# Kernel tuning notes

Hardware: AMD Instinct MI355X
Metric: run time of the kernel (lower is better)

Reference implementation:

```python
import jax, jax.numpy as jnp
import numpy as np

D_MODEL = 1024
N_HEAD = 16


def setup_inputs() -> dict:
    key = jax.random.key(0)
    ks = jax.random.split(key, 12)
    B, T, D = 2, 2048, D_MODEL
    s = 1.0 / np.sqrt(D)
    return {
        "q": jax.random.normal(ks[0], (B, T, D), jnp.float32),
        "k": jax.random.normal(ks[1], (B, T, D), jnp.float32),
        "v": jax.random.normal(ks[2], (B, T, D), jnp.float32),
        "w_q": jax.random.normal(ks[3], (D, D), jnp.float32) * s,
        "b_q": jnp.zeros((D,), jnp.float32),
        "w_k": jax.random.normal(ks[4], (D, D), jnp.float32) * s,
        "b_k": jnp.zeros((D,), jnp.float32),
        "w_v": jax.random.normal(ks[5], (D, D), jnp.float32) * s,
        "b_v": jnp.zeros((D,), jnp.float32),
        "w_o": jax.random.normal(ks[6], (D, D), jnp.float32) * s,
        "b_o": jnp.zeros((D,), jnp.float32),
    }


def reference(q, k, v, w_q, b_q, w_k, b_k, w_v, b_v, w_o, b_o):
    B, T, D = q.shape
    H = N_HEAD
    nd = D // H  # head dim
    # projections (weights stored as [in, out])
    qh = (q @ w_q + b_q).reshape(B, T, H, nd).transpose(0, 2, 1, 3)  # [b,h,t,nd]
    kh = (k @ w_k + b_k).reshape(B, T, H, nd).transpose(0, 2, 1, 3)
    vh = (v @ w_v + b_v).reshape(B, T, H, nd).transpose(0, 2, 1, 3)
    score = jnp.einsum('bhqd,bhkd->bhqk', qh, kh) / jnp.sqrt(jnp.float32(nd))
    causal = jnp.tril(jnp.ones((T, T), dtype=bool))  # [tq, tk]
    score = jnp.where(causal, score, -jnp.inf)
    # NOTE: original module uses nn.Softmax(dim=-2), i.e. softmax over the
    # QUERY axis. Faithful to the source.
    attn = jax.nn.softmax(score, axis=-2)
    out = jnp.einsum('bhqk,bhkd->bhqd', attn, vh)  # [b,h,t,nd]
    out = out.transpose(0, 2, 1, 3).reshape(B, T, D)
    return out @ w_o + b_o
```

## Files before the change

kernel.cpp:

```cpp
#include <hip/hip_runtime.h>
#include <hip/hip_bf16.h>
#include <cstdint>
#include <cstddef>

#define D_MODEL 1024
#define NHEAD   16
#define HDIM    64
#define BB      2
#define TT      2048
#define MM      (BB*TT)
#define BHN     (BB*NHEAD)

typedef __attribute__((ext_vector_type(8))) __bf16 bf16x8;
typedef __attribute__((ext_vector_type(4))) float  f32x4;
typedef __attribute__((ext_vector_type(8))) unsigned short u16x8;
typedef __attribute__((ext_vector_type(4))) unsigned short u16x4;

__device__ __forceinline__ unsigned short f2b(float f){
  __bf16 b = (__bf16)f;
  return __builtin_bit_cast(unsigned short, b);
}

__device__ __forceinline__ f32x4 mfma16(bf16x8 a, bf16x8 b, f32x4 c){
  return __builtin_amdgcn_mfma_f32_16x16x32_bf16(a, b, c, 0, 0, 0);
}

__device__ __forceinline__ void gload16(const void* g, void* lds){
  __builtin_amdgcn_global_load_lds((const __attribute__((address_space(1))) void*)g,
                                   (__attribute__((address_space(3))) void*)lds, 16, 0, 0);
}

__global__ void pre_kernel(const float* __restrict__ q, const float* __restrict__ k,
                           const float* __restrict__ v,
                           unsigned short* __restrict__ Xq, unsigned short* __restrict__ Xk,
                           unsigned short* __restrict__ Xv,
                           const float* __restrict__ W0, const float* __restrict__ W1,
                           const float* __restrict__ W2, const float* __restrict__ W3,
                           unsigned short* __restrict__ T0, unsigned short* __restrict__ T1,
                           unsigned short* __restrict__ T2, unsigned short* __restrict__ T3)
{
  __shared__ float tile[32][33];
  const int id = blockIdx.x;
  if (id < 6144){
    const int z = id / 2048, ib = id - z*2048;
    const float* x = z==0 ? q : z==1 ? k : v;
    unsigned short* y = z==0 ? Xq : z==1 ? Xk : Xv;
    size_t i = (size_t)ib*256 + threadIdx.x;
    const float4* p = (const float4*)(x + i*8);
    float4 a = p[0], b = p[1];
    u16x8 o;
    o[0]=f2b(a.x); o[1]=f2b(a.y); o[2]=f2b(a.z); o[3]=f2b(a.w);
    o[4]=f2b(b.x); o[5]=f2b(b.y); o[6]=f2b(b.z); o[7]=f2b(b.w);
    *(u16x8*)(y + i*8) = o;
  } else {
    const int tid = id - 6144;
    const int z = tid >> 10;
    const int by = (tid >> 5) & 31, bx = tid & 31;
    const float* W = z==0 ? W0 : z==1 ? W1 : z==2 ? W2 : W3;
    unsigned short* Wt = z==0 ? T0 : z==1 ? T1 : z==2 ? T2 : T3;
    const int tx = threadIdx.x & 31, ty = threadIdx.x >> 5;
    const int x0 = bx*32, y0 = by*32;
    #pragma unroll
    for (int i=0;i<4;i++)
      tile[ty + i*8][tx] = W[(size_t)(y0 + ty + i*8)*D_MODEL + x0 + tx];
    __syncthreads();
    #pragma unroll
    for (int i=0;i<4;i++)
      Wt[(size_t)(x0 + ty + i*8)*D_MODEL + y0 + tx] = f2b(tile[tx][ty + i*8]);
  }
}

__device__ __forceinline__ void gemm_body(const unsigned short* __restrict__ A,
                                          const unsigned short* __restrict__ Bt,
                                          const float* __restrict__ bias,
                                          void* __restrict__ Cout, const int mode,
                                          const int m0, const int n0)
{
  constexpr int K = D_MODEL, N = D_MODEL;
  __shared__ unsigned short As[2][128*32];
  __shared__ unsigned short Bs[2][128*32];
  const int t = threadIdx.x, lane = t&63, w = t>>6;
  const int wr = w>>1, wc = w&1, lr = lane&15, lg = lane>>4;
  const int srow = lane>>2;
  const int schunk = (lane&3) ^ ((lane>>3)&3);
  const int crd = lg ^ ((lr>>1)&3);
  f32x4 acc[4][4] = {};

  auto stage = [&](int buf, int k0){
    #pragma unroll
    for (int g=0; g<2; g++){
      int reg = w*2 + g;
      int r = reg*16 + srow;
      gload16(A  + (size_t)(m0+r)*K + k0 + schunk*8, (char*)As[buf] + reg*1024);
      gload16(Bt + (size_t)(n0+r)*K + k0 + schunk*8, (char*)Bs[buf] + reg*1024);
    }
  };

  stage(0, 0);
  __syncthreads();
  int buf = 0;
  for (int ks = 0; ks < 32; ++ks){
    if (ks < 31) stage(buf^1, (ks+1)*32);
    const char* bufA = (const char*)As[buf];
    const char* bufB = (const char*)Bs[buf];
    bf16x8 af[4], bfv[4];
    #pragma unroll
    for (int mi=0;mi<4;mi++){
      int r = wr*64 + mi*16 + lr;
      af[mi] = *(const bf16x8*)(bufA + r*64 + crd*16);
    }
    #pragma unroll
    for (int ni=0;ni<4;ni++){
      int r = wc*64 + ni*16 + lr;
      bfv[ni] = *(const bf16x8*)(bufB + r*64 + crd*16);
    }
    #pragma unroll
    for (int mi=0;mi<4;mi++)
      #pragma unroll
      for (int ni=0;ni<4;ni++)
        acc[mi][ni] = mfma16(af[mi], bfv[ni], acc[mi][ni]);
    __syncthreads();
    buf ^= 1;
  }

  #pragma unroll
  for (int mi=0;mi<4;mi++){
    #pragma unroll
    for (int ni=0;ni<4;ni++){
      int n = n0 + wc*64 + ni*16 + lr;
      int mbase = m0 + wr*64 + mi*16 + lg*4;
      float bv = bias[n];
      if (mode == 0){
        unsigned short* Cb = (unsigned short*)Cout;
        #pragma unroll
        for (int r=0;r<4;r++) Cb[(size_t)(mbase+r)*N + n] = f2b(acc[mi][ni][r] + bv);
      } else {
        unsigned short* Vt = (unsigned short*)Cout;
        int h = n >> 6, d = n & 63;
        int b = mbase >> 11;
        int tq = mbase & (TT-1);
        u16x4 vv;
        #pragma unroll
        for (int r=0;r<4;r++) vv[r] = f2b(acc[mi][ni][r] + bv);
        *(u16x4*)(Vt + ((size_t)((b*NHEAD + h)*HDIM + d))*TT + tq) = vv;
      }
    }
  }
}

__launch_bounds__(256)
__global__ void proj_gemm_kernel(const unsigned short* __restrict__ Xq,
                                 const unsigned short* __restrict__ Xk,
                                 const unsigned short* __restrict__ Xv,
                                 const unsigned short* __restrict__ Wtq,
                                 const unsigned short* __restrict__ Wtk,
                                 const unsigned short* __restrict__ Wtv,
                                 const float* __restrict__ b_q, const float* __restrict__ b_k,
                                 const float* __restrict__ b_v,
                                 unsigned short* __restrict__ Qb, unsigned short* __restrict__ Kb,
                                 unsigned short* __restrict__ Vt)
{
  const int id = blockIdx.x;
  const int xcd = id & 7, r2 = id >> 3;
  const int n = r2 & 7, mz = r2 >> 3;
  const int m = (mz & 3)*8 + xcd, z = mz >> 2;
  const unsigned short* A  = z==0 ? Xq : z==1 ? Xk : Xv;
  const unsigned short* Bt = z==0 ? Wtq : z==1 ? Wtk : Wtv;
  const float* bias = z==0 ? b_q : z==1 ? b_k : b_v;
  void* C = z==0 ? (void*)Qb : z==1 ? (void*)Kb : (void*)Vt;
  gemm_body(A, Bt, bias, C, z==2 ? 1 : 0, m*128, n*128);
}

__launch_bounds__(256)
__global__ void out_gemm_kernel(const unsigned short* __restrict__ Ob,
                                const unsigned short* __restrict__ Wto,
                                const float* __restrict__ b_o, float* __restrict__ out)
{
  constexpr int K = D_MODEL, N = D_MODEL;
  __shared__ unsigned short As[2][64*32];
  __shared__ unsigned short Bs[2][128*32];
  const int id = blockIdx.x;
  const int xcd = id & 7, r2 = id >> 3;
  const int n0 = (r2 & 7)*128, m0 = ((r2 >> 3)*8 + xcd)*64;
  const int t = threadIdx.x, lane = t&63, w = t>>6;
  const int wr = w>>1, wc = w&1, lr = lane&15, lg = lane>>4;
  const int srow = lane>>2;
  const int schunk = (lane&3) ^ ((lane>>3)&3);
  const int crd = lg ^ ((lr>>1)&3);
  f32x4 acc[2][4] = {};

  auto stage = [&](int buf, int k0){
    { int r = w*16 + srow;
      gload16(Ob + (size_t)(m0+r)*K + k0 + schunk*8, (char*)As[buf] + w*1024); }
    #pragma unroll
    for (int g=0; g<2; g++){
      int reg = w*2 + g;
      int r = reg*16 + srow;
      gload16(Wto + (size_t)(n0+r)*K + k0 + schunk*8, (char*)Bs[buf] + reg*1024);
    }
  };

  stage(0, 0);
  __syncthreads();
  int buf = 0;
  for (int ks = 0; ks < 32; ++ks){
    if (ks < 31) stage(buf^1, (ks+1)*32);
    const char* bufA = (const char*)As[buf];
    const char* bufB = (const char*)Bs[buf];
    bf16x8 af[2], bfv[4];
    #pragma unroll
    for (int mi=0;mi<2;mi++){
      int r = wr*32 + mi*16 + lr;
      af[mi] = *(const bf16x8*)(bufA + r*64 + crd*16);
    }
    #pragma unroll
    for (int ni=0;ni<4;ni++){
      int r = wc*64 + ni*16 + lr;
      bfv[ni] = *(const bf16x8*)(bufB + r*64 + crd*16);
    }
    #pragma unroll
    for (int mi=0;mi<2;mi++)
      #pragma unroll
      for (int ni=0;ni<4;ni++)
        acc[mi][ni] = mfma16(af[mi], bfv[ni], acc[mi][ni]);
    __syncthreads();
    buf ^= 1;
  }

  #pragma unroll
  for (int mi=0;mi<2;mi++){
    #pragma unroll
    for (int ni=0;ni<4;ni++){
      int n = n0 + wc*64 + ni*16 + lr;
      int mbase = m0 + wr*32 + mi*16 + lg*4;
      float bv = b_o[n];
      #pragma unroll
      for (int r=0;r<4;r++) out[(size_t)(mbase+r)*N + n] = acc[mi][ni][r] + bv;
    }
  }
}

__launch_bounds__(256)
__global__ void col_stats_kernel(const unsigned short* __restrict__ Qb,
                                 const unsigned short* __restrict__ Kb,
                                 float* __restrict__ partialS)
{
  __shared__ unsigned short Ks[128*64];
  __shared__ unsigned short Qs[2][64*64];
  const int t = threadIdx.x, lane = t&63, w = t>>6;
  const int id = blockIdx.x;
  const int bh = id & 31, pair = id >> 5;
  const int kb_ = pair & 15, qc = pair >> 4;
  const int b = bh >> 4, h = bh & 15;
  const int k0 = kb_ * 128;
  const int lr = lane&15, lg = lane>>4;
  const int osrc = (lane&7) ^ (lane>>3);

  auto stageQ = [&](int buf, int qt){
    #pragma unroll
    for (int g=0; g<2; g++){
      int reg = w*2 + g;
      int r = reg*8 + (lane>>3);
      gload16(Qb + ((size_t)(b*TT + qt + r))*D_MODEL + h*64 + osrc*8,
              (char*)Qs[buf] + reg*1024);
    }
  };

  const int qstart = (k0 > qc*256) ? k0 : qc*256;
  const int qend   = (qc+1)*256;

  #pragma unroll
  for (int g=0; g<4; g++){
    int reg = w*4 + g;
    int r = reg*8 + (lane>>3);
    gload16(Kb + ((size_t)(b*TT + k0 + r))*D_MODEL + h*64 + osrc*8, (char*)Ks + reg*1024);
  }
  if (qstart < qend) stageQ(0, qstart);
  __syncthreads();

  bf16x8 bk[2][2];
  #pragma unroll
  for (int kb=0;kb<2;kb++)
    #pragma unroll
    for (int ks=0;ks<2;ks++){
      int r = w*32 + kb*16 + lr;
      bk[kb][ks] = *(const bf16x8*)((const char*)Ks + r*128 + (((ks*4+lg) ^ (r&7))*16));
    }
  f32x4 sacc[2] = {};
  int buf = 0;
  for (int qt = qstart; qt < qend; qt += 64){
    if (qt + 64 < qend) stageQ(buf^1, qt+64);
    const char* bufQ = (const char*)Qs[buf];
    const bool interior = (qt >= k0 + 128);
    #pragma unroll
    for (int qb=0;qb<4;qb++){
      bf16x8 aq[2];
      #pragma unroll
      for (int ks=0;ks<2;ks++){
        int r = qb*16 + lr;
        aq[ks] = *(const bf16x8*)(bufQ + r*128 + (((ks*4+lg) ^ (r&7))*16));
      }
      f32x4 sf[2] = {};
      #pragma unroll
      for (int ks=0;ks<2;ks++)
        #pragma unroll
        for (int kb=0;kb<2;kb++)
          sf[kb] = mfma16(aq[ks], bk[kb][ks], sf[kb]);
      #pragma unroll
      for (int kb=0;kb<2;kb++){
        int col = k0 + w*32 + kb*16 + lr;
        #pragma unroll
        for (int r=0;r<4;r++){
          float e = __expf(sf[kb][r] * 0.125f);
          if (!interior){
            int qg = qt + qb*16 + lg*4 + r;
            e = (qg >= col) ? e : 0.f;
          }
          sacc[kb][r] += e;
        }
      }
    }
    __syncthreads();
    buf ^= 1;
  }
  #pragma unroll
  for (int kb=0;kb<2;kb++){
    float s = sacc[kb][0] + sacc[kb][1] + sacc[kb][2] + sacc[kb][3];
    s += __shfl_xor(s, 16);
    s += __shfl_xor(s, 32);
    if (lg == 0){
      int col = k0 + w*32 + kb*16 + lr;
      partialS[((size_t)qc*BHN + bh)*TT + col] = s;
    }
  }
}

__launch_bounds__(512)
__global__ void attn_out_kernel(const unsigned short* __restrict__ Qb,
                                const unsigned short* __restrict__ Kb,
                                const unsigned short* __restrict__ Vt,
                                const float* __restrict__ partialS,
                                unsigned short* __restrict__ O)
{
  __shared__ unsigned short Qs[128*64];
  __shared__ unsigned short Ks2[2][64*64];
  __shared__ unsigned short Vs[2][64*64];
  __shared__ unsigned short Ps[128*64];
  __shared__ float inv_s[TT];
  const int t = threadIdx.x, lane=t&63, w=t>>6;
  const int id = blockIdx.x;
  const int bh = id & 31;
  const int qi = 15 - (id >> 5);
  const int b = bh>>4, h = bh&15;
  const int q0 = qi*128;
  const int lr = lane&15, lg = lane>>4;
  const int osrc = (lane&7) ^ (lane>>3);

  auto stageKV = [&](int buf, int k0){
    int r = w*8 + (lane>>3);
    gload16(Kb + ((size_t)(b*TT + k0 + r))*D_MODEL + h*64 + osrc*8,
            (char*)Ks2[buf] + w*1024);
    gload16(Vt + ((size_t)(bh*HDIM + r))*TT + k0 + osrc*8,
            (char*)Vs[buf] + w*1024);
  };

  #pragma unroll
  for (int g=0; g<2; g++){
    int reg = w*2 + g;
    int r = reg*8 + (lane>>3);
    gload16(Qb + ((size_t)(b*TT + q0 + r))*D_MODEL + h*64 + osrc*8, (char*)Qs + reg*1024);
  }
  stageKV(0, 0);

  const int ncols = q0 + 128;
  for (int c = t; c < ncols; c += 512){
    float s = 0.f;
    #pragma unroll
    for (int qc=0;qc<8;qc++) s += partialS[((size_t)qc*BHN + bh)*TT + c];
    inv_s[c] = 1.0f / s;
  }
  __syncthreads();

  bf16x8 aq[2];
  #pragma unroll
  for (int ks=0;ks<2;ks++){
    int r = w*16 + lr;
    aq[ks] = *(const bf16x8*)((const char*)Qs + r*128 + (((ks*4+lg) ^ (r&7))*16));
  }
  f32x4 oacc[4] = {};
  const int nkt = 2*qi + 2;
  int buf = 0;
  for (int kt=0; kt<nkt; kt++){
    int k0 = kt*64;
    if (kt+1 < nkt) stageKV(buf^1, k0+64);
    const bool active = (k0 <= q0 + w*16 + 15);
    if (active){
      const char* bufK = (const char*)Ks2[buf];
      const char* bufV = (const char*)Vs[buf];
      f32x4 sf[4] = {};
      __builtin_amdgcn_s_setprio(1);
      #pragma unroll
      for (int ks=0;ks<2;ks++)
        #pragma unroll
        for (int kb=0;kb<4;kb++){
          int r = kb*16 + lr;
          bf16x8 bk = *(const bf16x8*)(bufK + r*128 + (((ks*4+lg) ^ (r&7))*16));
          sf[kb] = mfma16(bk, aq[ks], sf[kb]);
        }
      __builtin_amdgcn_s_setprio(0);
      const bool boundary = (k0 + 64 > q0 + w*16);
      const int prow = w*16 + lr;
      #pragma unroll
      for (int kb=0;kb<4;kb++){
        f32x4 inv4 = *(const f32x4*)&inv_s[k0 + kb*16 + lg*4];
        u16x4 vv;
        #pragma unroll
        for (int r=0;r<4;r++){
          float pv = __expf(sf[kb][r]*0.125f) * inv4[r];
          if (boundary){
            int kg = k0 + kb*16 + lg*4 + r;
            int qg = q0 + prow;
            pv = (qg >= kg) ? pv : 0.f;
          }
          vv[r] = f2b(pv);
        }
        *(u16x4*)((char*)Ps + ((prow*128 + kb*32 + lg*8) ^ ((prow&7)<<4))) = vv;
      }
      __builtin_amdgcn_s_setprio(1);
      #pragma unroll
      for (int ks=0;ks<2;ks++){
        bf16x8 pa = *(const bf16x8*)((const char*)Ps + prow*128 + (((ks*4+lg) ^ (prow&7))*16));
        #pragma unroll
        for (int db=0;db<4;db++){
          int r = db*16 + lr;
          bf16x8 bv = *(const bf16x8*)(bufV + r*128 + (((ks*4+lg) ^ (r&7))*16));
          oacc[db] = mfma16(pa, bv, oacc[db]);
        }
      }
      __builtin_amdgcn_s_setprio(0);
    }
    __syncthreads();
    buf ^= 1;
  }
  #pragma unroll
  for (int db=0;db<4;db++){
    int qg = q0 + w*16 + lg*4;
    int d  = db*16 + lr;
    #pragma unroll
    for (int r=0;r<4;r++)
      O[((size_t)(b*TT + qg + r))*D_MODEL + h*64 + d] = f2b(oacc[db][r]);
  }
}

extern "C" void kernel_launch(void* const* d_in, const int* in_sizes, int n_in,
                              void* d_out, int out_size, void* d_ws, size_t ws_size,
                              hipStream_t stream)
{
  (void)in_sizes; (void)n_in; (void)out_size; (void)ws_size;
  const float* q   = (const float*)d_in[0];
  const float* k   = (const float*)d_in[1];
  const float* v   = (const float*)d_in[2];
  const float* w_q = (const float*)d_in[3];
  const float* b_q = (const float*)d_in[4];
  const float* w_k = (const float*)d_in[5];
  const float* b_k = (const float*)d_in[6];
  const float* w_v = (const float*)d_in[7];
  const float* b_v = (const float*)d_in[8];
  const float* w_o = (const float*)d_in[9];
  const float* b_o = (const float*)d_in[10];

  char* p = (char*)d_ws;
  auto carve = [&](size_t bytes)->char* {
    char* r = p; p += (bytes + 255) & ~(size_t)255; return r;
  };
  unsigned short* Xq  = (unsigned short*)carve((size_t)MM*D_MODEL*2);
  unsigned short* Xk  = (unsigned short*)carve((size_t)MM*D_MODEL*2);
  unsigned short* Xv  = (unsigned short*)carve((size_t)MM*D_MODEL*2);
  unsigned short* Wtq = (unsigned short*)carve((size_t)D_MODEL*D_MODEL*2);
  unsigned short* Wtk = (unsigned short*)carve((size_t)D_MODEL*D_MODEL*2);
  unsigned short* Wtv = (unsigned short*)carve((size_t)D_MODEL*D_MODEL*2);
  unsigned short* Wto = (unsigned short*)carve((size_t)D_MODEL*D_MODEL*2);
  unsigned short* Qb  = (unsigned short*)carve((size_t)MM*D_MODEL*2);
  unsigned short* Kb  = (unsigned short*)carve((size_t)MM*D_MODEL*2);
  unsigned short* Vt  = (unsigned short*)carve((size_t)MM*D_MODEL*2);
  unsigned short* Ob  = (unsigned short*)carve((size_t)MM*D_MODEL*2);
  float* partialS = (float*)carve((size_t)8*BHN*TT*4);

  pre_kernel<<<dim3(6144 + 4096), 256, 0, stream>>>(q, k, v, Xq, Xk, Xv,
                                                    w_q, w_k, w_v, w_o,
                                                    Wtq, Wtk, Wtv, Wto);

  proj_gemm_kernel<<<dim3(768), 256, 0, stream>>>(Xq, Xk, Xv, Wtq, Wtk, Wtv,
                                                  b_q, b_k, b_v, Qb, Kb, Vt);

  col_stats_kernel<<<dim3(8*16*BHN), 256, 0, stream>>>(Qb, Kb, partialS);

  attn_out_kernel<<<dim3((TT/128)*BHN), 512, 0, stream>>>(Qb, Kb, Vt, partialS, Ob);

  out_gemm_kernel<<<dim3(512), 256, 0, stream>>>(Ob, Wto, b_o, (float*)d_out);
}
```

Baseline: 142.6 us.

## Pair causal query strips per block for balanced attention and fold score scale into Q

The attention-output kernel now gives each 256-thread block two 64-row query strips, one near the start and its mirror near the end, so every block covers the same number of causal key tiles and shares each staged K/V tile between both strips. The 1/sqrt(d) scale is applied once when Q is written in the projection GEMM, which removes a multiply from the exp in both the column-stats and attention kernels. This trades 512-thread blocks with idle warps for balanced smaller blocks. It also rounds the scaled Q to bf16, which changes numerics slightly.

```diff
diff --git a/kernel.cpp b/kernel.cpp
--- a/kernel.cpp
+++ b/kernel.cpp
@@ -74,7 +74,7 @@
                                           const unsigned short* __restrict__ Bt,
                                           const float* __restrict__ bias,
                                           void* __restrict__ Cout, const int mode,
-                                          const int m0, const int n0)
+                                          const int m0, const int n0, const float oscale)
 {
   constexpr int K = D_MODEL, N = D_MODEL;
   __shared__ unsigned short As[2][128*32];
@@ -133,7 +133,7 @@
       if (mode == 0){
         unsigned short* Cb = (unsigned short*)Cout;
         #pragma unroll
-        for (int r=0;r<4;r++) Cb[(size_t)(mbase+r)*N + n] = f2b(acc[mi][ni][r] + bv);
+        for (int r=0;r<4;r++) Cb[(size_t)(mbase+r)*N + n] = f2b((acc[mi][ni][r] + bv)*oscale);
       } else {
         unsigned short* Vt = (unsigned short*)Cout;
         int h = n >> 6, d = n & 63;
@@ -168,7 +168,7 @@
   const unsigned short* Bt = z==0 ? Wtq : z==1 ? Wtk : Wtv;
   const float* bias = z==0 ? b_q : z==1 ? b_k : b_v;
   void* C = z==0 ? (void*)Qb : z==1 ? (void*)Kb : (void*)Vt;
-  gemm_body(A, Bt, bias, C, z==2 ? 1 : 0, m*128, n*128);
+  gemm_body(A, Bt, bias, C, z==2 ? 1 : 0, m*128, n*128, z==0 ? 0.125f : 1.0f);
 }
 
 __launch_bounds__(256)
@@ -311,7 +311,7 @@
         int col = k0 + w*32 + kb*16 + lr;
         #pragma unroll
         for (int r=0;r<4;r++){
-          float e = __expf(sf[kb][r] * 0.125f);
+          float e = __expf(sf[kb][r]);
           if (!interior){
             int qg = qt + qb*16 + lg*4 + r;
             e = (qg >= col) ? e : 0.f;
@@ -335,45 +335,55 @@
   }
 }
 
-__launch_bounds__(512)
+__launch_bounds__(256)
 __global__ void attn_out_kernel(const unsigned short* __restrict__ Qb,
                                 const unsigned short* __restrict__ Kb,
                                 const unsigned short* __restrict__ Vt,
                                 const float* __restrict__ partialS,
                                 unsigned short* __restrict__ O)
 {
-  __shared__ unsigned short Qs[128*64];
+  __shared__ unsigned short Qs[2][64*64];
   __shared__ unsigned short Ks2[2][64*64];
   __shared__ unsigned short Vs[2][64*64];
-  __shared__ unsigned short Ps[128*64];
+  __shared__ unsigned short Ps[64*64];
   __shared__ float inv_s[TT];
   const int t = threadIdx.x, lane=t&63, w=t>>6;
   const int id = blockIdx.x;
   const int bh = id & 31;
-  const int qi = 15 - (id >> 5);
+  const int pr = id >> 5;
   const int b = bh>>4, h = bh&15;
-  const int q0 = qi*128;
+  const int q0A = pr*64, q0B = (31-pr)*64;
+  const int nkt = (31-pr) + 1;
   const int lr = lane&15, lg = lane>>4;
   const int osrc = (lane&7) ^ (lane>>3);
 
+  auto stageQ = [&](int s, int q0){
+    #pragma unroll
+    for (int g=0; g<2; g++){
+      int reg = w*2 + g;
+      int r = reg*8 + (lane>>3);
+      gload16(Qb + ((size_t)(b*TT + q0 + r))*D_MODEL + h*64 + osrc*8,
+              (char*)Qs[s] + reg*1024);
+    }
+  };
   auto stageKV = [&](int buf, int k0){
-    int r = w*8 + (lane>>3);
-    gload16(Kb + ((size_t)(b*TT + k0 + r))*D_MODEL + h*64 + osrc*8,
-            (char*)Ks2[buf] + w*1024);
-    gload16(Vt + ((size_t)(bh*HDIM + r))*TT + k0 + osrc*8,
-            (char*)Vs[buf] + w*1024);
-  };
-
-  #pragma unroll
-  for (int g=0; g<2; g++){
-    int reg = w*2 + g;
-    int r = reg*8 + (lane>>3);
-    gload16(Qb + ((size_t)(b*TT + q0 + r))*D_MODEL + h*64 + osrc*8, (char*)Qs + reg*1024);
-  }
+    #pragma unroll
+    for (int g=0; g<2; g++){
+      int reg = w*2 + g;
+      int r = reg*8 + (lane>>3);
+      gload16(Kb + ((size_t)(b*TT + k0 + r))*D_MODEL + h*64 + osrc*8,
+              (char*)Ks2[buf] + reg*1024);
+      gload16(Vt + ((size_t)(bh*HDIM + r))*TT + k0 + osrc*8,
+              (char*)Vs[buf] + reg*1024);
+    }
+  };
+
+  stageQ(0, q0A);
+  stageQ(1, q0B);
   stageKV(0, 0);
 
-  const int ncols = q0 + 128;
-  for (int c = t; c < ncols; c += 512){
+  const int ncols = nkt*64;
+  for (int c = t; c < ncols; c += 256){
     float s = 0.f;
     #pragma unroll
     for (int qc=0;qc<8;qc++) s += partialS[((size_t)qc*BHN + bh)*TT + c];
@@ -381,74 +391,81 @@
   }
   __syncthreads();
 
-  bf16x8 aq[2];
+  bf16x8 aqA[2], aqB[2];
   #pragma unroll
   for (int ks=0;ks<2;ks++){
     int r = w*16 + lr;
-    aq[ks] = *(const bf16x8*)((const char*)Qs + r*128 + (((ks*4+lg) ^ (r&7))*16));
-  }
-  f32x4 oacc[4] = {};
-  const int nkt = 2*qi + 2;
+    aqA[ks] = *(const bf16x8*)((const char*)Qs[0] + r*128 + (((ks*4+lg) ^ (r&7))*16));
+    aqB[ks] = *(const bf16x8*)((const char*)Qs[1] + r*128 + (((ks*4+lg) ^ (r&7))*16));
+  }
+  f32x4 oaccA[4] = {}, oaccB[4] = {};
+  const int prow = w*16 + lr;
+
+  auto strip_step = [&](const bf16x8* aq, f32x4* oacc, int q0, int k0,
+                        const char* bufK, const char* bufV){
+    f32x4 sf[4] = {};
+    __builtin_amdgcn_s_setprio(1);
+    #pragma unroll
+    for (int ks=0;ks<2;ks++)
+      #pragma unroll
+      for (int kb=0;kb<4;kb++){
+        int r = kb*16 + lr;
+        bf16x8 bk = *(const bf16x8*)(bufK + r*128 + (((ks*4+lg) ^ (r&7))*16));
+        sf[kb] = mfma16(bk, aq[ks], sf[kb]);
+      }
+    __builtin_amdgcn_s_setprio(0);
+    const bool boundary = (k0 + 64 > q0 + w*16);
+    #pragma unroll
+    for (int kb=0;kb<4;kb++){
+      f32x4 inv4 = *(const f32x4*)&inv_s[k0 + kb*16 + lg*4];
+      u16x4 vv;
+      #pragma unroll
+      for (int r=0;r<4;r++){
+        float pv = __expf(sf[kb][r]) * inv4[r];
+        if (boundary){
+          int kg = k0 + kb*16 + lg*4 + r;
+          pv = (q0 + prow >= kg) ? pv : 0.f;
+        }
+        vv[r] = f2b(pv);
+      }
+      *(u16x4*)((char*)Ps + ((prow*128 + kb*32 + lg*8) ^ ((prow&7)<<4))) = vv;
+    }
+    __builtin_amdgcn_s_setprio(1);
+    #pragma unroll
+    for (int ks=0;ks<2;ks++){
+      bf16x8 pa = *(const bf16x8*)((const char*)Ps + prow*128 + (((ks*4+lg) ^ (prow&7))*16));
+      #pragma unroll
+      for (int db=0;db<4;db++){
+        int r = db*16 + lr;
+        bf16x8 bv = *(const bf16x8*)(bufV + r*128 + (((ks*4+lg) ^ (r&7))*16));
+        oacc[db] = mfma16(pa, bv, oacc[db]);
+      }
+    }
+    __builtin_amdgcn_s_setprio(0);
+  };
+
   int buf = 0;
   for (int kt=0; kt<nkt; kt++){
     int k0 = kt*64;
     if (kt+1 < nkt) stageKV(buf^1, k0+64);
-    const bool active = (k0 <= q0 + w*16 + 15);
-    if (active){
-      const char* bufK = (const char*)Ks2[buf];
-      const char* bufV = (const char*)Vs[buf];
-      f32x4 sf[4] = {};
-      __builtin_amdgcn_s_setprio(1);
-      #pragma unroll
-      for (int ks=0;ks<2;ks++)
-        #pragma unroll
-        for (int kb=0;kb<4;kb++){
-          int r = kb*16 + lr;
-          bf16x8 bk = *(const bf16x8*)(bufK + r*128 + (((ks*4+lg) ^ (r&7))*16));
-          sf[kb] = mfma16(bk, aq[ks], sf[kb]);
-        }
-      __builtin_amdgcn_s_setprio(0);
-      const bool boundary = (k0 + 64 > q0 + w*16);
-      const int prow = w*16 + lr;
-      #pragma unroll
-      for (int kb=0;kb<4;kb++){
-        f32x4 inv4 = *(const f32x4*)&inv_s[k0 + kb*16 + lg*4];
-        u16x4 vv;
-        #pragma unroll
-        for (int r=0;r<4;r++){
-          float pv = __expf(sf[kb][r]*0.125f) * inv4[r];
-          if (boundary){
-            int kg = k0 + kb*16 + lg*4 + r;
-            int qg = q0 + prow;
-            pv = (qg >= kg) ? pv : 0.f;
-          }
-          vv[r] = f2b(pv);
-        }
-        *(u16x4*)((char*)Ps + ((prow*128 + kb*32 + lg*8) ^ ((prow&7)<<4))) = vv;
-      }
-      __builtin_amdgcn_s_setprio(1);
-      #pragma unroll
-      for (int ks=0;ks<2;ks++){
-        bf16x8 pa = *(const bf16x8*)((const char*)Ps + prow*128 + (((ks*4+lg) ^ (prow&7))*16));
-        #pragma unroll
-        for (int db=0;db<4;db++){
-          int r = db*16 + lr;
-          bf16x8 bv = *(const bf16x8*)(bufV + r*128 + (((ks*4+lg) ^ (r&7))*16));
-          oacc[db] = mfma16(pa, bv, oacc[db]);
-        }
-      }
-      __builtin_amdgcn_s_setprio(0);
-    }
+    const char* bufK = (const char*)Ks2[buf];
+    const char* bufV = (const char*)Vs[buf];
+    if (k0 <= q0A + w*16 + 15)
+      strip_step(aqA, oaccA, q0A, k0, bufK, bufV);
+    strip_step(aqB, oaccB, q0B, k0, bufK, bufV);
     __syncthreads();
     buf ^= 1;
   }
   #pragma unroll
   for (int db=0;db<4;db++){
-    int qg = q0 + w*16 + lg*4;
-    int d  = db*16 + lr;
-    #pragma unroll
-    for (int r=0;r<4;r++)
-      O[((size_t)(b*TT + qg + r))*D_MODEL + h*64 + d] = f2b(oacc[db][r]);
+    int d = db*16 + lr;
+    int qgA = q0A + w*16 + lg*4;
+    int qgB = q0B + w*16 + lg*4;
+    #pragma unroll
+    for (int r=0;r<4;r++){
+      O[((size_t)(b*TT + qgA + r))*D_MODEL + h*64 + d] = f2b(oaccA[db][r]);
+      O[((size_t)(b*TT + qgB + r))*D_MODEL + h*64 + d] = f2b(oaccB[db][r]);
+    }
   }
 }
 
@@ -495,7 +512,7 @@
 
   col_stats_kernel<<<dim3(8*16*BHN), 256, 0, stream>>>(Qb, Kb, partialS);
 
-  attn_out_kernel<<<dim3((TT/128)*BHN), 512, 0, stream>>>(Qb, Kb, Vt, partialS, Ob);
+  attn_out_kernel<<<dim3(16*BHN), 256, 0, stream>>>(Qb, Kb, Vt, partialS, Ob);
 
   out_gemm_kernel<<<dim3(512), 256, 0, stream>>>(Ob, Wto, b_o, (float*)d_out);
 }
```

After: 141.6 us. No clear change (-0.7%).

## Fold softmax scale into Q projection, precombine column sums, shrink attention tiles

Applied to the files above, without the earlier changes.

The 1/sqrt(d) scale is folded into the Q projection epilogue, which removes a multiply before each exp in both attention kernels. A new small kernel reduces the per-chunk partial column sums into reciprocals once, so each attention block no longer recomputes them into shared memory. The attention output kernel moves from 128-query tiles with 512 threads to 64-query tiles with 256 threads, which doubles the grid and drops the per-warp causal skip branch. In exchange there is an extra launch, the reciprocals are read from global memory inside the loop, and scaling Q before the bf16 rounding changes numerics slightly.

```diff
diff --git a/kernel.cpp b/kernel.cpp
--- a/kernel.cpp
+++ b/kernel.cpp
@@ -74,7 +74,7 @@
                                           const unsigned short* __restrict__ Bt,
                                           const float* __restrict__ bias,
                                           void* __restrict__ Cout, const int mode,
-                                          const int m0, const int n0)
+                                          const int m0, const int n0, const float oscale)
 {
   constexpr int K = D_MODEL, N = D_MODEL;
   __shared__ unsigned short As[2][128*32];
@@ -133,7 +133,7 @@
       if (mode == 0){
         unsigned short* Cb = (unsigned short*)Cout;
         #pragma unroll
-        for (int r=0;r<4;r++) Cb[(size_t)(mbase+r)*N + n] = f2b(acc[mi][ni][r] + bv);
+        for (int r=0;r<4;r++) Cb[(size_t)(mbase+r)*N + n] = f2b((acc[mi][ni][r] + bv)*oscale);
       } else {
         unsigned short* Vt = (unsigned short*)Cout;
         int h = n >> 6, d = n & 63;
@@ -168,7 +168,7 @@
   const unsigned short* Bt = z==0 ? Wtq : z==1 ? Wtk : Wtv;
   const float* bias = z==0 ? b_q : z==1 ? b_k : b_v;
   void* C = z==0 ? (void*)Qb : z==1 ? (void*)Kb : (void*)Vt;
-  gemm_body(A, Bt, bias, C, z==2 ? 1 : 0, m*128, n*128);
+  gemm_body(A, Bt, bias, C, z==2 ? 1 : 0, m*128, n*128, z==0 ? 0.125f : 1.0f);
 }
 
 __launch_bounds__(256)
@@ -311,7 +311,7 @@
         int col = k0 + w*32 + kb*16 + lr;
         #pragma unroll
         for (int r=0;r<4;r++){
-          float e = __expf(sf[kb][r] * 0.125f);
+          float e = __expf(sf[kb][r]);
           if (!interior){
             int qg = qt + qb*16 + lg*4 + r;
             e = (qg >= col) ? e : 0.f;
@@ -335,33 +335,45 @@
   }
 }
 
-__launch_bounds__(512)
+__global__ void col_combine_kernel(const float* __restrict__ partialS,
+                                   float* __restrict__ colS){
+  int i = blockIdx.x*256 + threadIdx.x;
+  float s = 0.f;
+  #pragma unroll
+  for (int qc=0;qc<8;qc++) s += partialS[(size_t)qc*BHN*TT + i];
+  colS[i] = 1.0f / s;
+}
+
+__launch_bounds__(256)
 __global__ void attn_out_kernel(const unsigned short* __restrict__ Qb,
                                 const unsigned short* __restrict__ Kb,
                                 const unsigned short* __restrict__ Vt,
-                                const float* __restrict__ partialS,
+                                const float* __restrict__ colS,
                                 unsigned short* __restrict__ O)
 {
-  __shared__ unsigned short Qs[128*64];
+  __shared__ unsigned short Qs[64*64];
   __shared__ unsigned short Ks2[2][64*64];
   __shared__ unsigned short Vs[2][64*64];
-  __shared__ unsigned short Ps[128*64];
-  __shared__ float inv_s[TT];
+  __shared__ unsigned short Ps[64*64];
   const int t = threadIdx.x, lane=t&63, w=t>>6;
   const int id = blockIdx.x;
   const int bh = id & 31;
-  const int qi = 15 - (id >> 5);
+  const int qi = 31 - (id >> 5);
   const int b = bh>>4, h = bh&15;
-  const int q0 = qi*128;
+  const int q0 = qi*64;
   const int lr = lane&15, lg = lane>>4;
   const int osrc = (lane&7) ^ (lane>>3);
 
   auto stageKV = [&](int buf, int k0){
-    int r = w*8 + (lane>>3);
-    gload16(Kb + ((size_t)(b*TT + k0 + r))*D_MODEL + h*64 + osrc*8,
-            (char*)Ks2[buf] + w*1024);
-    gload16(Vt + ((size_t)(bh*HDIM + r))*TT + k0 + osrc*8,
-            (char*)Vs[buf] + w*1024);
+    #pragma unroll
+    for (int g=0; g<2; g++){
+      int reg = w*2 + g;
+      int r = reg*8 + (lane>>3);
+      gload16(Kb + ((size_t)(b*TT + k0 + r))*D_MODEL + h*64 + osrc*8,
+              (char*)Ks2[buf] + reg*1024);
+      gload16(Vt + ((size_t)(bh*HDIM + r))*TT + k0 + osrc*8,
+              (char*)Vs[buf] + reg*1024);
+    }
   };
 
   #pragma unroll
@@ -371,14 +383,6 @@
     gload16(Qb + ((size_t)(b*TT + q0 + r))*D_MODEL + h*64 + osrc*8, (char*)Qs + reg*1024);
   }
   stageKV(0, 0);
-
-  const int ncols = q0 + 128;
-  for (int c = t; c < ncols; c += 512){
-    float s = 0.f;
-    #pragma unroll
-    for (int qc=0;qc<8;qc++) s += partialS[((size_t)qc*BHN + bh)*TT + c];
-    inv_s[c] = 1.0f / s;
-  }
   __syncthreads();
 
   bf16x8 aq[2];
@@ -388,57 +392,53 @@
     aq[ks] = *(const bf16x8*)((const char*)Qs + r*128 + (((ks*4+lg) ^ (r&7))*16));
   }
   f32x4 oacc[4] = {};
-  const int nkt = 2*qi + 2;
+  const int nkt = qi + 1;
+  const int prow = w*16 + lr;
   int buf = 0;
   for (int kt=0; kt<nkt; kt++){
     int k0 = kt*64;
     if (kt+1 < nkt) stageKV(buf^1, k0+64);
-    const bool active = (k0 <= q0 + w*16 + 15);
-    if (active){
-      const char* bufK = (const char*)Ks2[buf];
-      const char* bufV = (const char*)Vs[buf];
-      f32x4 sf[4] = {};
-      __builtin_amdgcn_s_setprio(1);
-      #pragma unroll
-      for (int ks=0;ks<2;ks++)
-        #pragma unroll
-        for (int kb=0;kb<4;kb++){
-          int r = kb*16 + lr;
-          bf16x8 bk = *(const bf16x8*)(bufK + r*128 + (((ks*4+lg) ^ (r&7))*16));
-          sf[kb] = mfma16(bk, aq[ks], sf[kb]);
+    const char* bufK = (const char*)Ks2[buf];
+    const char* bufV = (const char*)Vs[buf];
+    f32x4 sf[4] = {};
+    __builtin_amdgcn_s_setprio(1);
+    #pragma unroll
+    for (int ks=0;ks<2;ks++)
+      #pragma unroll
+      for (int kb=0;kb<4;kb++){
+        int r = kb*16 + lr;
+        bf16x8 bk = *(const bf16x8*)(bufK + r*128 + (((ks*4+lg) ^ (r&7))*16));
+        sf[kb] = mfma16(bk, aq[ks], sf[kb]);
+      }
+    __builtin_amdgcn_s_setprio(0);
+    const bool boundary = (k0 + 64 > q0 + w*16);
+    #pragma unroll
+    for (int kb=0;kb<4;kb++){
+      f32x4 inv4 = *(const f32x4*)(colS + (size_t)bh*TT + k0 + kb*16 + lg*4);
+      u16x4 vv;
+      #pragma unroll
+      for (int r=0;r<4;r++){
+        float pv = __expf(sf[kb][r]) * inv4[r];
+        if (boundary){
+          int kg = k0 + kb*16 + lg*4 + r;
+          pv = (q0 + prow >= kg) ? pv : 0.f;
         }
-      __builtin_amdgcn_s_setprio(0);
-      const bool boundary = (k0 + 64 > q0 + w*16);
-      const int prow = w*16 + lr;
-      #pragma unroll
-      for (int kb=0;kb<4;kb++){
-        f32x4 inv4 = *(const f32x4*)&inv_s[k0 + kb*16 + lg*4];
-        u16x4 vv;
-        #pragma unroll
-        for (int r=0;r<4;r++){
-          float pv = __expf(sf[kb][r]*0.125f) * inv4[r];
-          if (boundary){
-            int kg = k0 + kb*16 + lg*4 + r;
-            int qg = q0 + prow;
-            pv = (qg >= kg) ? pv : 0.f;
-          }
-          vv[r] = f2b(pv);
-        }
-        *(u16x4*)((char*)Ps + ((prow*128 + kb*32 + lg*8) ^ ((prow&7)<<4))) = vv;
+        vv[r] = f2b(pv);
       }
-      __builtin_amdgcn_s_setprio(1);
-      #pragma unroll
-      for (int ks=0;ks<2;ks++){
-        bf16x8 pa = *(const bf16x8*)((const char*)Ps + prow*128 + (((ks*4+lg) ^ (prow&7))*16));
-        #pragma unroll
-        for (int db=0;db<4;db++){
-          int r = db*16 + lr;
-          bf16x8 bv = *(const bf16x8*)(bufV + r*128 + (((ks*4+lg) ^ (r&7))*16));
-          oacc[db] = mfma16(pa, bv, oacc[db]);
-        }
+      *(u16x4*)((char*)Ps + ((prow*128 + kb*32 + lg*8) ^ ((prow&7)<<4))) = vv;
+    }
+    __builtin_amdgcn_s_setprio(1);
+    #pragma unroll
+    for (int ks=0;ks<2;ks++){
+      bf16x8 pa = *(const bf16x8*)((const char*)Ps + prow*128 + (((ks*4+lg) ^ (prow&7))*16));
+      #pragma unroll
+      for (int db=0;db<4;db++){
+        int r = db*16 + lr;
+        bf16x8 bv = *(const bf16x8*)(bufV + r*128 + (((ks*4+lg) ^ (r&7))*16));
+        oacc[db] = mfma16(pa, bv, oacc[db]);
       }
-      __builtin_amdgcn_s_setprio(0);
-    }
+    }
+    __builtin_amdgcn_s_setprio(0);
     __syncthreads();
     buf ^= 1;
   }
@@ -485,6 +485,7 @@
   unsigned short* Vt  = (unsigned short*)carve((size_t)MM*D_MODEL*2);
   unsigned short* Ob  = (unsigned short*)carve((size_t)MM*D_MODEL*2);
   float* partialS = (float*)carve((size_t)8*BHN*TT*4);
+  float* colS     = (float*)carve((size_t)BHN*TT*4);
 
   pre_kernel<<<dim3(6144 + 4096), 256, 0, stream>>>(q, k, v, Xq, Xk, Xv,
                                                     w_q, w_k, w_v, w_o,
@@ -494,8 +495,9 @@
                                                   b_q, b_k, b_v, Qb, Kb, Vt);
 
   col_stats_kernel<<<dim3(8*16*BHN), 256, 0, stream>>>(Qb, Kb, partialS);
-
-  attn_out_kernel<<<dim3((TT/128)*BHN), 512, 0, stream>>>(Qb, Kb, Vt, partialS, Ob);
+  col_combine_kernel<<<dim3(BHN*TT/256), 256, 0, stream>>>(partialS, colS);
+
+  attn_out_kernel<<<dim3(32*BHN), 256, 0, stream>>>(Qb, Kb, Vt, colS, Ob);
 
   out_gemm_kernel<<<dim3(512), 256, 0, stream>>>(Ob, Wto, b_o, (float*)d_out);
 }
```

Measured after the change: 144.7 us. Within noise of the previous version (+1.5%).
